# Optimization experiments

Hardware: AMD Instinct MI355X
Metric: run time of the kernel (lower is better)

Reference implementation:

```python
import jax, jax.numpy as jnp
import numpy as np

N_NODES = 100000
N_EDGES = 1600000
D_IN = 64
D_OUT = 64


def setup_inputs() -> dict:
    key = jax.random.key(0)
    k1, k2, k3, k4 = jax.random.split(key, 4)
    x = jax.random.normal(k1, (N_NODES, D_IN), dtype=jnp.float32)
    edge_index = jax.random.randint(k2, (2, N_EDGES), 0, N_NODES, dtype=jnp.int64)
    W = jax.random.normal(k3, (D_OUT, D_IN), dtype=jnp.float32) * (1.0 / np.sqrt(D_IN))
    b = jax.random.normal(k4, (D_OUT,), dtype=jnp.float32) * 0.01
    return {"x": x, "edge_index": edge_index, "W": W, "b": b}


def reference(x, edge_index, W, b):
    num_nodes = x.shape[0]
    row, col = edge_index[0], edge_index[1]
    # degree of each node as a destination (scatter_add of ones over row)
    deg = jax.ops.segment_sum(jnp.ones(row.shape[0], dtype=x.dtype), row,
                              num_segments=num_nodes)
    # deg^-0.5 with inf (deg==0) replaced by 0
    deg_inv_sqrt = jnp.where(deg > 0, jax.lax.rsqrt(jnp.maximum(deg, 1.0)) * jnp.where(deg > 0, 1.0, 0.0), 0.0)
    deg_inv_sqrt = jnp.where(deg > 0, deg ** -0.5, 0.0)
    # gather source features, scale by source norm, scatter-add to destinations
    weighted = x[col] * deg_inv_sqrt[col][:, None]          # [E, D_IN]
    agg = jax.ops.segment_sum(weighted, row, num_segments=num_nodes)  # [N, D_IN]
    agg = agg * deg_inv_sqrt[:, None]
    # linear + relu (torch Linear: y = agg @ W.T + b)
    return jax.nn.relu(agg @ W.T + b)
```

## Files before the change

kernel.cpp:

```cpp
#include <hip/hip_runtime.h>

#define N_NODES 100000
#define N_EDGES 1600000
#define D 64

#define FSHIFT 5
#define FNODES 32
#define NFB 3125
#define CAPF 800

#define CSHIFT 11
#define NCB 49
#define CCAP 36864
#define FPC 64
#define NCHUNKB 9

#define CHUNK 4096
#define EPT 16
#define NCHUNKA 391

#define COLBITS 17
#define COLMASK 0x1FFFF

#define FCUR_OFF   0
#define CCUR_OFF   16384
#define CPAIRS_OFF 32768
#define FPAIRS_OFF 7258112
#define Y_OFF      17258112

typedef float fvec4 __attribute__((ext_vector_type(4)));

__device__ __forceinline__ float bf2f(unsigned short u) {
    return __uint_as_float(((unsigned)u) << 16);
}
__device__ __forceinline__ unsigned f2bf(float f) {
    unsigned bits = __float_as_uint(f);
    return (bits + 0x7FFFu + ((bits >> 16) & 1u)) >> 16;
}

__global__ void initcur_kernel(int* __restrict__ fcur, int* __restrict__ ccur) {
    int i = blockIdx.x * blockDim.x + threadIdx.x;
    if (i < NFB) fcur[i] = i * CAPF;
    if (i < NCB) ccur[i] = i * CCAP;
}

__global__ __launch_bounds__(256) void scatA_kernel(const int* __restrict__ row,
                                                    const int* __restrict__ col,
                                                    int* __restrict__ ccur,
                                                    int* __restrict__ cpairs) {
    __shared__ int lcnt[NCB];
    int t = threadIdx.x;
    int base = blockIdx.x * CHUNK;
    if (t < NCB) lcnt[t] = 0;
    __syncthreads();
    int r[EPT], c[EPT], pos[EPT];
#pragma unroll
    for (int i = 0; i < EPT; ++i) {
        int e = base + i * 256 + t;
        if (e < N_EDGES) {
            r[i] = row[e];
            c[i] = col[e];
            pos[i] = atomicAdd(&lcnt[r[i] >> CSHIFT], 1);
        } else r[i] = -1;
    }
    __syncthreads();
    if (t < NCB) {
        int cc = lcnt[t];
        if (cc) lcnt[t] = atomicAdd(&ccur[t], cc);
    }
    __syncthreads();
#pragma unroll
    for (int i = 0; i < EPT; ++i) {
        if (r[i] >= 0) {
            int cb = r[i] >> CSHIFT;
            int rl = r[i] & ((1 << CSHIFT) - 1);
            cpairs[lcnt[cb] + pos[i]] = (rl << COLBITS) | c[i];
        }
    }
}

__global__ __launch_bounds__(256) void scatB_kernel(const int* __restrict__ cpairs,
                                                    const int* __restrict__ ccur,
                                                    int* __restrict__ fcur,
                                                    int* __restrict__ fpairs) {
    __shared__ int lcnt[FPC];
    int t = threadIdx.x;
    int cb = blockIdx.x / NCHUNKB;
    int k  = blockIdx.x % NCHUNKB;
    int beg = cb * CCAP + k * CHUNK;
    int end = ccur[cb];
    if (end > beg + CHUNK) end = beg + CHUNK;
    if (t < FPC) lcnt[t] = 0;
    __syncthreads();
    int pc[EPT], pos[EPT];
#pragma unroll
    for (int i = 0; i < EPT; ++i) {
        int e = beg + i * 256 + t;
        if (e < end) {
            pc[i] = cpairs[e];
            pos[i] = atomicAdd(&lcnt[pc[i] >> (COLBITS + FSHIFT)], 1);
        } else pc[i] = -1;
    }
    __syncthreads();
    if (t < FPC) {
        int cc = lcnt[t];
        if (cc) lcnt[t] = atomicAdd(&fcur[(cb << 6) + t], cc);
    }
    __syncthreads();
#pragma unroll
    for (int i = 0; i < EPT; ++i) {
        if (pc[i] >= 0) {
            int fl = pc[i] >> (COLBITS + FSHIFT);
            int rl5 = (pc[i] >> COLBITS) & (FNODES - 1);
            fpairs[lcnt[fl] + pos[i]] = (rl5 << COLBITS) | (pc[i] & COLMASK);
        }
    }
}

__global__ __launch_bounds__(256) void xform_kernel(
        const float* __restrict__ x, const float* __restrict__ W,
        const int* __restrict__ fpairs, const int* __restrict__ fcur,
        unsigned short* __restrict__ y) {
    __shared__ __align__(16) float XT[D * 68];
    __shared__ __align__(16) float WT[D * 68];
    __shared__ int hist[64];
    __shared__ float dl[64];
    int t = threadIdx.x;
    int b = blockIdx.x;
    int nb0 = b << 6;
    for (int i = t; i < D * D; i += 256) {
        int j = i >> 6, d = i & 63;
        WT[d * 68 + j] = W[i];
    }
    if (t < 64) hist[t] = 0;
    __syncthreads();
    for (int i = t; i < 64 * D; i += 256) {
        int n = i >> 6, d = i & 63;
        int g = nb0 + n;
        XT[d * 68 + n] = (g < N_NODES) ? x[(size_t)g * D + d] : 0.0f;
    }
#pragma unroll
    for (int half = 0; half < 2; ++half) {
        int f = 2 * b + half;
        if (f < NFB) {
            int beg = f * CAPF, end = fcur[f];
            for (int k = beg + t; k < end; k += 256)
                atomicAdd(&hist[(fpairs[k] >> COLBITS) + (half << FSHIFT)], 1);
        }
    }
    __syncthreads();
    if (t < 64) dl[t] = (hist[t] > 0) ? rsqrtf((float)hist[t]) : 0.0f;
    __syncthreads();
    int tj = t & 15, tn = t >> 4;
    float4 a0 = {0,0,0,0}, a1 = {0,0,0,0}, a2 = {0,0,0,0}, a3 = {0,0,0,0};
#pragma unroll 8
    for (int d = 0; d < D; ++d) {
        float4 xv = *(const float4*)&XT[d * 68 + tn * 4];
        float4 wv = *(const float4*)&WT[d * 68 + tj * 4];
        a0.x = fmaf(xv.x, wv.x, a0.x); a0.y = fmaf(xv.x, wv.y, a0.y);
        a0.z = fmaf(xv.x, wv.z, a0.z); a0.w = fmaf(xv.x, wv.w, a0.w);
        a1.x = fmaf(xv.y, wv.x, a1.x); a1.y = fmaf(xv.y, wv.y, a1.y);
        a1.z = fmaf(xv.y, wv.z, a1.z); a1.w = fmaf(xv.y, wv.w, a1.w);
        a2.x = fmaf(xv.z, wv.x, a2.x); a2.y = fmaf(xv.z, wv.y, a2.y);
        a2.z = fmaf(xv.z, wv.z, a2.z); a2.w = fmaf(xv.z, wv.w, a2.w);
        a3.x = fmaf(xv.w, wv.x, a3.x); a3.y = fmaf(xv.w, wv.y, a3.y);
        a3.z = fmaf(xv.w, wv.z, a3.z); a3.w = fmaf(xv.w, wv.w, a3.w);
    }
    int jb = tj * 4;
#pragma unroll
    for (int s = 0; s < 4; ++s) {
        int g = nb0 + tn * 4 + s;
        if (g < N_NODES) {
            float sc = dl[tn * 4 + s];
            float4 a = (s == 0) ? a0 : (s == 1) ? a1 : (s == 2) ? a2 : a3;
            unsigned lo = f2bf(a.x * sc) | (f2bf(a.y * sc) << 16);
            unsigned hi = f2bf(a.z * sc) | (f2bf(a.w * sc) << 16);
            *(uint2*)(y + (size_t)g * D + jb) = make_uint2(lo, hi);
        }
    }
}

__global__ __launch_bounds__(256) void mega_kernel(
        const int* __restrict__ fpairs, const int* __restrict__ fcur,
        const unsigned short* __restrict__ y,
        const float* __restrict__ bias, float* __restrict__ out) {
    __shared__ int hist[FNODES];
    __shared__ int sc[FNODES];
    __shared__ int lrptr[FNODES + 1];
    __shared__ int lcur[FNODES];
    __shared__ float dl[FNODES];
    __shared__ int lds_scol[CAPF];
    int t = threadIdx.x;
    int b = blockIdx.x;
    int beg = b * CAPF, end = fcur[b];
    if (t < FNODES) hist[t] = 0;
    __syncthreads();
    for (int k = beg + t; k < end; k += 256)
        atomicAdd(&hist[fpairs[k] >> COLBITS], 1);
    __syncthreads();
    if (t < FNODES) sc[t] = hist[t];
    __syncthreads();
    for (int off = 1; off < FNODES; off <<= 1) {
        int v = (t < FNODES && t >= off) ? sc[t - off] : 0;
        __syncthreads();
        if (t < FNODES) sc[t] += v;
        __syncthreads();
    }
    if (t < FNODES) {
        lrptr[t + 1] = sc[t];
        lcur[t] = sc[t] - hist[t];
        dl[t] = (hist[t] > 0) ? rsqrtf((float)hist[t]) : 0.0f;
    }
    if (t == 0) lrptr[0] = 0;
    __syncthreads();
    for (int k = beg + t; k < end; k += 256) {
        int p = fpairs[k];
        int pos = atomicAdd(&lcur[p >> COLBITS], 1);
        lds_scol[pos] = p & COLMASK;
    }
    __syncthreads();
    int wave = t >> 6;
    int lane = t & 63;
    int g = lane >> 3;
    int q = lane & 7;
    float bj[8];
    {
        float4 b0 = *(const float4*)(bias + q * 8);
        float4 b1 = *(const float4*)(bias + q * 8 + 4);
        bj[0] = b0.x; bj[1] = b0.y; bj[2] = b0.z; bj[3] = b0.w;
        bj[4] = b1.x; bj[5] = b1.y; bj[6] = b1.z; bj[7] = b1.w;
    }
    for (int ln = wave; ln < FNODES; ln += 4) {
        int s = lrptr[ln], e2 = lrptr[ln + 1];
        float a[8];
#pragma unroll
        for (int i = 0; i < 8; ++i) a[i] = 0.0f;
        for (int k = s; k < e2; k += 32) {
#pragma unroll
            for (int u = 0; u < 4; ++u) {
                int e = k + u * 8 + g;
                if (e < e2) {
                    int c = lds_scol[e];
                    uint4 v = *(const uint4*)(y + (size_t)c * D + q * 8);
                    a[0] += __uint_as_float(v.x << 16);
                    a[1] += __uint_as_float(v.x & 0xffff0000u);
                    a[2] += __uint_as_float(v.y << 16);
                    a[3] += __uint_as_float(v.y & 0xffff0000u);
                    a[4] += __uint_as_float(v.z << 16);
                    a[5] += __uint_as_float(v.z & 0xffff0000u);
                    a[6] += __uint_as_float(v.w << 16);
                    a[7] += __uint_as_float(v.w & 0xffff0000u);
                }
            }
        }
#pragma unroll
        for (int m = 8; m <= 32; m <<= 1) {
#pragma unroll
            for (int i = 0; i < 8; ++i)
                a[i] += __shfl_xor(a[i], m);
        }
        float dv = dl[ln];
        int n = (b << FSHIFT) + ln;
        if (g < 2) {
            int o = g * 4;
            fvec4 r;
            r.x = fmaxf(fmaf(dv, a[o + 0], bj[o + 0]), 0.0f);
            r.y = fmaxf(fmaf(dv, a[o + 1], bj[o + 1]), 0.0f);
            r.z = fmaxf(fmaf(dv, a[o + 2], bj[o + 2]), 0.0f);
            r.w = fmaxf(fmaf(dv, a[o + 3], bj[o + 3]), 0.0f);
            __builtin_nontemporal_store(r, (fvec4*)(out + (size_t)n * D + q * 8 + o));
        }
    }
}

extern "C" void kernel_launch(void* const* d_in, const int* in_sizes, int n_in,
                              void* d_out, int out_size, void* d_ws, size_t ws_size,
                              hipStream_t stream) {
    const float* x    = (const float*)d_in[0];
    const int*   eidx = (const int*)d_in[1];
    const float* W    = (const float*)d_in[2];
    const float* b    = (const float*)d_in[3];
    float* out = (float*)d_out;
    char* ws = (char*)d_ws;

    const int* row = eidx;
    const int* col = eidx + N_EDGES;

    int* fcur   = (int*)(ws + FCUR_OFF);
    int* ccur   = (int*)(ws + CCUR_OFF);
    int* cpairs = (int*)(ws + CPAIRS_OFF);
    int* fpairs = (int*)(ws + FPAIRS_OFF);
    unsigned short* y = (unsigned short*)(ws + Y_OFF);

    initcur_kernel<<<(NFB + 255) / 256, 256, 0, stream>>>(fcur, ccur);
    scatA_kernel<<<NCHUNKA, 256, 0, stream>>>(row, col, ccur, cpairs);
    scatB_kernel<<<NCB * NCHUNKB, 256, 0, stream>>>(cpairs, ccur, fcur, fpairs);
    xform_kernel<<<(N_NODES + 63) / 64, 256, 0, stream>>>(x, W, fpairs, fcur, y);
    mega_kernel<<<NFB, 256, 0, stream>>>(fpairs, fcur, y, b, out);
}
```

Before: 183.8 us.

## Split feature gather into column planes with a separate CSR prep kernel

```diff
diff --git a/kernel.cpp b/kernel.cpp
--- a/kernel.cpp
+++ b/kernel.cpp
@@ -7,41 +7,39 @@
 #define FSHIFT 5
 #define FNODES 32
 #define NFB 3125
-#define CAPF 800
+#define CAPF 768
 
 #define CSHIFT 11
 #define NCB 49
 #define CCAP 36864
 #define FPC 64
-#define NCHUNKB 9
-
-#define CHUNK 4096
-#define EPT 16
-#define NCHUNKA 391
+
+#define CHUNKA 2048
+#define EPTA 8
+#define NCHUNKA 782
+#define CHUNKB 2048
+#define EPTB 8
+#define NCHUNKB 18
 
 #define COLBITS 17
 #define COLMASK 0x1FFFF
 
-#define FCUR_OFF   0
-#define CCUR_OFF   16384
-#define CPAIRS_OFF 32768
-#define FPAIRS_OFF 7258112
-#define Y_OFF      17258112
+#define PLANE_B 1600000
+
+#define CCUR_OFF   0
+#define FCUR_OFF   4096
+#define INIT_BYTES 16640
+#define RPTR_OFF   16640
+#define DINV_OFF   429312
+#define Y_OFF      829440
+#define FPAIRS_OFF 13629440
+#define SORT_OFF   23229440
 
 typedef float fvec4 __attribute__((ext_vector_type(4)));
 
-__device__ __forceinline__ float bf2f(unsigned short u) {
-    return __uint_as_float(((unsigned)u) << 16);
-}
 __device__ __forceinline__ unsigned f2bf(float f) {
     unsigned bits = __float_as_uint(f);
     return (bits + 0x7FFFu + ((bits >> 16) & 1u)) >> 16;
-}
-
-__global__ void initcur_kernel(int* __restrict__ fcur, int* __restrict__ ccur) {
-    int i = blockIdx.x * blockDim.x + threadIdx.x;
-    if (i < NFB) fcur[i] = i * CAPF;
-    if (i < NCB) ccur[i] = i * CCAP;
 }
 
 __global__ __launch_bounds__(256) void scatA_kernel(const int* __restrict__ row,
@@ -50,12 +48,12 @@
                                                     int* __restrict__ cpairs) {
     __shared__ int lcnt[NCB];
     int t = threadIdx.x;
-    int base = blockIdx.x * CHUNK;
+    int base = blockIdx.x * CHUNKA;
     if (t < NCB) lcnt[t] = 0;
     __syncthreads();
-    int r[EPT], c[EPT], pos[EPT];
-#pragma unroll
-    for (int i = 0; i < EPT; ++i) {
+    int r[EPTA], c[EPTA], pos[EPTA];
+#pragma unroll
+    for (int i = 0; i < EPTA; ++i) {
         int e = base + i * 256 + t;
         if (e < N_EDGES) {
             r[i] = row[e];
@@ -66,11 +64,11 @@
     __syncthreads();
     if (t < NCB) {
         int cc = lcnt[t];
-        if (cc) lcnt[t] = atomicAdd(&ccur[t], cc);
-    }
-    __syncthreads();
-#pragma unroll
-    for (int i = 0; i < EPT; ++i) {
+        if (cc) lcnt[t] = t * CCAP + atomicAdd(&ccur[t], cc);
+    }
+    __syncthreads();
+#pragma unroll
+    for (int i = 0; i < EPTA; ++i) {
         if (r[i] >= 0) {
             int cb = r[i] >> CSHIFT;
             int rl = r[i] & ((1 << CSHIFT) - 1);
@@ -87,14 +85,14 @@
     int t = threadIdx.x;
     int cb = blockIdx.x / NCHUNKB;
     int k  = blockIdx.x % NCHUNKB;
-    int beg = cb * CCAP + k * CHUNK;
-    int end = ccur[cb];
-    if (end > beg + CHUNK) end = beg + CHUNK;
+    int beg = cb * CCAP + k * CHUNKB;
+    int end = cb * CCAP + ccur[cb];
+    if (end > beg + CHUNKB) end = beg + CHUNKB;
     if (t < FPC) lcnt[t] = 0;
     __syncthreads();
-    int pc[EPT], pos[EPT];
-#pragma unroll
-    for (int i = 0; i < EPT; ++i) {
+    int pc[EPTB], pos[EPTB];
+#pragma unroll
+    for (int i = 0; i < EPTB; ++i) {
         int e = beg + i * 256 + t;
         if (e < end) {
             pc[i] = cpairs[e];
@@ -104,11 +102,14 @@
     __syncthreads();
     if (t < FPC) {
         int cc = lcnt[t];
-        if (cc) lcnt[t] = atomicAdd(&fcur[(cb << 6) + t], cc);
-    }
-    __syncthreads();
-#pragma unroll
-    for (int i = 0; i < EPT; ++i) {
+        if (cc) {
+            int fb = (cb << 6) + t;
+            lcnt[t] = fb * CAPF + atomicAdd(&fcur[fb], cc);
+        }
+    }
+    __syncthreads();
+#pragma unroll
+    for (int i = 0; i < EPTB; ++i) {
         if (pc[i] >= 0) {
             int fl = pc[i] >> (COLBITS + FSHIFT);
             int rl5 = (pc[i] >> COLBITS) & (FNODES - 1);
@@ -117,14 +118,55 @@
     }
 }
 
+__global__ __launch_bounds__(256) void binprep_kernel(
+        const int* __restrict__ fpairs, const int* __restrict__ fcur,
+        int* __restrict__ sorted, int* __restrict__ rptr,
+        float* __restrict__ dinv) {
+    __shared__ int hist[FNODES];
+    __shared__ int sc[FNODES];
+    __shared__ int lcur[FNODES];
+    __shared__ int lds_scol[CAPF];
+    int t = threadIdx.x;
+    int f = blockIdx.x;
+    int beg = f * CAPF;
+    int cnt = fcur[f];
+    if (t < FNODES) hist[t] = 0;
+    __syncthreads();
+    for (int k = t; k < cnt; k += 256)
+        atomicAdd(&hist[fpairs[beg + k] >> COLBITS], 1);
+    __syncthreads();
+    if (t < FNODES) sc[t] = hist[t];
+    __syncthreads();
+    for (int off = 1; off < FNODES; off <<= 1) {
+        int v = (t < FNODES && t >= off) ? sc[t - off] : 0;
+        __syncthreads();
+        if (t < FNODES) sc[t] += v;
+        __syncthreads();
+    }
+    if (t < FNODES) {
+        int start = sc[t] - hist[t];
+        lcur[t] = start;
+        rptr[f * 33 + t] = beg + start;
+        int n = (f << FSHIFT) + t;
+        dinv[n] = (hist[t] > 0) ? rsqrtf((float)hist[t]) : 0.0f;
+    }
+    if (t == 0) rptr[f * 33 + 32] = beg + cnt;
+    __syncthreads();
+    for (int k = t; k < cnt; k += 256) {
+        int p = fpairs[beg + k];
+        int pos = atomicAdd(&lcur[p >> COLBITS], 1);
+        lds_scol[pos] = p & COLMASK;
+    }
+    __syncthreads();
+    for (int k = t; k < cnt; k += 256)
+        sorted[beg + k] = lds_scol[k];
+}
+
 __global__ __launch_bounds__(256) void xform_kernel(
         const float* __restrict__ x, const float* __restrict__ W,
-        const int* __restrict__ fpairs, const int* __restrict__ fcur,
-        unsigned short* __restrict__ y) {
+        const float* __restrict__ dinv, char* __restrict__ yb) {
     __shared__ __align__(16) float XT[D * 68];
     __shared__ __align__(16) float WT[D * 68];
-    __shared__ int hist[64];
-    __shared__ float dl[64];
     int t = threadIdx.x;
     int b = blockIdx.x;
     int nb0 = b << 6;
@@ -132,24 +174,11 @@
         int j = i >> 6, d = i & 63;
         WT[d * 68 + j] = W[i];
     }
-    if (t < 64) hist[t] = 0;
-    __syncthreads();
     for (int i = t; i < 64 * D; i += 256) {
         int n = i >> 6, d = i & 63;
         int g = nb0 + n;
         XT[d * 68 + n] = (g < N_NODES) ? x[(size_t)g * D + d] : 0.0f;
     }
-#pragma unroll
-    for (int half = 0; half < 2; ++half) {
-        int f = 2 * b + half;
-        if (f < NFB) {
-            int beg = f * CAPF, end = fcur[f];
-            for (int k = beg + t; k < end; k += 256)
-                atomicAdd(&hist[(fpairs[k] >> COLBITS) + (half << FSHIFT)], 1);
-        }
-    }
-    __syncthreads();
-    if (t < 64) dl[t] = (hist[t] > 0) ? rsqrtf((float)hist[t]) : 0.0f;
     __syncthreads();
     int tj = t & 15, tn = t >> 4;
     float4 a0 = {0,0,0,0}, a1 = {0,0,0,0}, a2 = {0,0,0,0}, a3 = {0,0,0,0};
@@ -166,109 +195,88 @@
         a3.x = fmaf(xv.w, wv.x, a3.x); a3.y = fmaf(xv.w, wv.y, a3.y);
         a3.z = fmaf(xv.w, wv.z, a3.z); a3.w = fmaf(xv.w, wv.w, a3.w);
     }
-    int jb = tj * 4;
+    int p = tj >> 1, half = tj & 1;
 #pragma unroll
     for (int s = 0; s < 4; ++s) {
         int g = nb0 + tn * 4 + s;
         if (g < N_NODES) {
-            float sc = dl[tn * 4 + s];
+            float scv = dinv[g];
             float4 a = (s == 0) ? a0 : (s == 1) ? a1 : (s == 2) ? a2 : a3;
-            unsigned lo = f2bf(a.x * sc) | (f2bf(a.y * sc) << 16);
-            unsigned hi = f2bf(a.z * sc) | (f2bf(a.w * sc) << 16);
-            *(uint2*)(y + (size_t)g * D + jb) = make_uint2(lo, hi);
-        }
-    }
-}
-
-__global__ __launch_bounds__(256) void mega_kernel(
-        const int* __restrict__ fpairs, const int* __restrict__ fcur,
-        const unsigned short* __restrict__ y,
+            unsigned lo = f2bf(a.x * scv) | (f2bf(a.y * scv) << 16);
+            unsigned hi = f2bf(a.z * scv) | (f2bf(a.w * scv) << 16);
+            *(uint2*)(yb + (size_t)p * PLANE_B + (size_t)g * 16 + half * 8) =
+                make_uint2(lo, hi);
+        }
+    }
+}
+
+__global__ __launch_bounds__(256) void gather_kernel(
+        const int* __restrict__ sorted, const int* __restrict__ rptr,
+        const float* __restrict__ dinv, const char* __restrict__ yb,
         const float* __restrict__ bias, float* __restrict__ out) {
-    __shared__ int hist[FNODES];
-    __shared__ int sc[FNODES];
-    __shared__ int lrptr[FNODES + 1];
-    __shared__ int lcur[FNODES];
-    __shared__ float dl[FNODES];
-    __shared__ int lds_scol[CAPF];
-    int t = threadIdx.x;
-    int b = blockIdx.x;
-    int beg = b * CAPF, end = fcur[b];
-    if (t < FNODES) hist[t] = 0;
-    __syncthreads();
-    for (int k = beg + t; k < end; k += 256)
-        atomicAdd(&hist[fpairs[k] >> COLBITS], 1);
-    __syncthreads();
-    if (t < FNODES) sc[t] = hist[t];
-    __syncthreads();
-    for (int off = 1; off < FNODES; off <<= 1) {
-        int v = (t < FNODES && t >= off) ? sc[t - off] : 0;
-        __syncthreads();
-        if (t < FNODES) sc[t] += v;
-        __syncthreads();
-    }
-    if (t < FNODES) {
-        lrptr[t + 1] = sc[t];
-        lcur[t] = sc[t] - hist[t];
-        dl[t] = (hist[t] > 0) ? rsqrtf((float)hist[t]) : 0.0f;
-    }
-    if (t == 0) lrptr[0] = 0;
-    __syncthreads();
-    for (int k = beg + t; k < end; k += 256) {
-        int p = fpairs[k];
-        int pos = atomicAdd(&lcur[p >> COLBITS], 1);
-        lds_scol[pos] = p & COLMASK;
-    }
-    __syncthreads();
-    int wave = t >> 6;
+    int blk = blockIdx.x;
+    int f = blk >> 3;
+    int s = blk & 7;
+    int t = threadIdx.x;
+    int w = t >> 6;
     int lane = t & 63;
-    int g = lane >> 3;
-    int q = lane & 7;
+    int ln2 = lane >> 4;
+    int g = lane & 15;
+    const char* yp = yb + (size_t)s * PLANE_B;
     float bj[8];
     {
-        float4 b0 = *(const float4*)(bias + q * 8);
-        float4 b1 = *(const float4*)(bias + q * 8 + 4);
+        float4 b0 = *(const float4*)(bias + s * 8);
+        float4 b1 = *(const float4*)(bias + s * 8 + 4);
         bj[0] = b0.x; bj[1] = b0.y; bj[2] = b0.z; bj[3] = b0.w;
         bj[4] = b1.x; bj[5] = b1.y; bj[6] = b1.z; bj[7] = b1.w;
     }
-    for (int ln = wave; ln < FNODES; ln += 4) {
-        int s = lrptr[ln], e2 = lrptr[ln + 1];
+    int nb0 = f << FSHIFT;
+#pragma unroll
+    for (int round = 0; round < 2; ++round) {
+        int ln = w * 8 + round * 4 + ln2;
+        int seg = rptr[f * 33 + ln];
+        int deg = rptr[f * 33 + ln + 1] - seg;
+        int md = deg;
+        md = max(md, __shfl_xor(md, 16));
+        md = max(md, __shfl_xor(md, 32));
         float a[8];
 #pragma unroll
         for (int i = 0; i < 8; ++i) a[i] = 0.0f;
-        for (int k = s; k < e2; k += 32) {
-#pragma unroll
-            for (int u = 0; u < 4; ++u) {
-                int e = k + u * 8 + g;
-                if (e < e2) {
-                    int c = lds_scol[e];
-                    uint4 v = *(const uint4*)(y + (size_t)c * D + q * 8);
-                    a[0] += __uint_as_float(v.x << 16);
-                    a[1] += __uint_as_float(v.x & 0xffff0000u);
-                    a[2] += __uint_as_float(v.y << 16);
-                    a[3] += __uint_as_float(v.y & 0xffff0000u);
-                    a[4] += __uint_as_float(v.z << 16);
-                    a[5] += __uint_as_float(v.z & 0xffff0000u);
-                    a[6] += __uint_as_float(v.w << 16);
-                    a[7] += __uint_as_float(v.w & 0xffff0000u);
-                }
+        for (int base = 0; base < md; base += 16) {
+            int o = base + g;
+            if (o < deg) {
+                int c = sorted[seg + o];
+                uint4 v = *(const uint4*)(yp + (size_t)c * 16);
+                a[0] += __uint_as_float(v.x << 16);
+                a[1] += __uint_as_float(v.x & 0xffff0000u);
+                a[2] += __uint_as_float(v.y << 16);
+                a[3] += __uint_as_float(v.y & 0xffff0000u);
+                a[4] += __uint_as_float(v.z << 16);
+                a[5] += __uint_as_float(v.z & 0xffff0000u);
+                a[6] += __uint_as_float(v.w << 16);
+                a[7] += __uint_as_float(v.w & 0xffff0000u);
             }
         }
 #pragma unroll
-        for (int m = 8; m <= 32; m <<= 1) {
+        for (int m = 1; m <= 8; m <<= 1) {
 #pragma unroll
             for (int i = 0; i < 8; ++i)
                 a[i] += __shfl_xor(a[i], m);
         }
-        float dv = dl[ln];
-        int n = (b << FSHIFT) + ln;
-        if (g < 2) {
-            int o = g * 4;
-            fvec4 r;
-            r.x = fmaxf(fmaf(dv, a[o + 0], bj[o + 0]), 0.0f);
-            r.y = fmaxf(fmaf(dv, a[o + 1], bj[o + 1]), 0.0f);
-            r.z = fmaxf(fmaf(dv, a[o + 2], bj[o + 2]), 0.0f);
-            r.w = fmaxf(fmaf(dv, a[o + 3], bj[o + 3]), 0.0f);
-            __builtin_nontemporal_store(r, (fvec4*)(out + (size_t)n * D + q * 8 + o));
+        if (g == 0) {
+            int n = nb0 + ln;
+            float dv = dinv[n];
+            fvec4 r0, r1;
+            r0.x = fmaxf(fmaf(dv, a[0], bj[0]), 0.0f);
+            r0.y = fmaxf(fmaf(dv, a[1], bj[1]), 0.0f);
+            r0.z = fmaxf(fmaf(dv, a[2], bj[2]), 0.0f);
+            r0.w = fmaxf(fmaf(dv, a[3], bj[3]), 0.0f);
+            r1.x = fmaxf(fmaf(dv, a[4], bj[4]), 0.0f);
+            r1.y = fmaxf(fmaf(dv, a[5], bj[5]), 0.0f);
+            r1.z = fmaxf(fmaf(dv, a[6], bj[6]), 0.0f);
+            r1.w = fmaxf(fmaf(dv, a[7], bj[7]), 0.0f);
+            __builtin_nontemporal_store(r0, (fvec4*)(out + (size_t)n * D + s * 8));
+            __builtin_nontemporal_store(r1, (fvec4*)(out + (size_t)n * D + s * 8 + 4));
         }
     }
 }
@@ -286,15 +294,19 @@
     const int* row = eidx;
     const int* col = eidx + N_EDGES;
 
-    int* fcur   = (int*)(ws + FCUR_OFF);
-    int* ccur   = (int*)(ws + CCUR_OFF);
-    int* cpairs = (int*)(ws + CPAIRS_OFF);
-    int* fpairs = (int*)(ws + FPAIRS_OFF);
-    unsigned short* y = (unsigned short*)(ws + Y_OFF);
-
-    initcur_kernel<<<(NFB + 255) / 256, 256, 0, stream>>>(fcur, ccur);
+    int*   ccur   = (int*)  (ws + CCUR_OFF);
+    int*   fcur   = (int*)  (ws + FCUR_OFF);
+    int*   rptr   = (int*)  (ws + RPTR_OFF);
+    float* dinv   = (float*)(ws + DINV_OFF);
+    char*  yb     =          ws + Y_OFF;
+    int*   fpairs = (int*)  (ws + FPAIRS_OFF);
+    int*   sorted = (int*)  (ws + SORT_OFF);
+    int*   cpairs = (int*)  (ws + SORT_OFF);
+
+    hipMemsetAsync(ws + CCUR_OFF, 0, INIT_BYTES, stream);
     scatA_kernel<<<NCHUNKA, 256, 0, stream>>>(row, col, ccur, cpairs);
     scatB_kernel<<<NCB * NCHUNKB, 256, 0, stream>>>(cpairs, ccur, fcur, fpairs);
-    xform_kernel<<<(N_NODES + 63) / 64, 256, 0, stream>>>(x, W, fpairs, fcur, y);
-    mega_kernel<<<NFB, 256, 0, stream>>>(fpairs, fcur, y, b, out);
-}
+    binprep_kernel<<<NFB, 256, 0, stream>>>(fpairs, fcur, sorted, rptr, dinv);
+    xform_kernel<<<(N_NODES + 63) / 64, 256, 0, stream>>>(x, W, dinv, yb);
+    gather_kernel<<<NFB * 8, 256, 0, stream>>>(sorted, rptr, dinv, yb, b, out);
+}
```

Result: slower. 240.6 us (+30.9%).

## Compute degree norms in scatter pass and split binning counters per wave

Applied to the files above, without the earlier changes.

```diff
diff --git a/kernel.cpp b/kernel.cpp
--- a/kernel.cpp
+++ b/kernel.cpp
@@ -7,123 +7,155 @@
 #define FSHIFT 5
 #define FNODES 32
 #define NFB 3125
-#define CAPF 800
+#define CAPF 768
 
 #define CSHIFT 11
+#define CNODES 2048
 #define NCB 49
 #define CCAP 36864
 #define FPC 64
-#define NCHUNKB 9
-
-#define CHUNK 4096
-#define EPT 16
+
+#define CHUNKA 4096
+#define EPTA 16
 #define NCHUNKA 391
+#define CHUNKB 2048
+#define EPTB 8
+#define NCHUNKB 18
 
 #define COLBITS 17
 #define COLMASK 0x1FFFF
 
-#define FCUR_OFF   0
-#define CCUR_OFF   16384
-#define CPAIRS_OFF 32768
-#define FPAIRS_OFF 7258112
-#define Y_OFF      17258112
+#define CCUR_OFF   0
+#define FCUR_OFF   256
+#define INIT_BYTES 12756
+#define DINV_OFF   16384
+#define Y_OFF      417792
+#define CPAIRS_OFF 13217792
+#define FPAIRS_OFF 20443136
 
 typedef float fvec4 __attribute__((ext_vector_type(4)));
 
-__device__ __forceinline__ float bf2f(unsigned short u) {
-    return __uint_as_float(((unsigned)u) << 16);
-}
 __device__ __forceinline__ unsigned f2bf(float f) {
     unsigned bits = __float_as_uint(f);
     return (bits + 0x7FFFu + ((bits >> 16) & 1u)) >> 16;
-}
-
-__global__ void initcur_kernel(int* __restrict__ fcur, int* __restrict__ ccur) {
-    int i = blockIdx.x * blockDim.x + threadIdx.x;
-    if (i < NFB) fcur[i] = i * CAPF;
-    if (i < NCB) ccur[i] = i * CCAP;
 }
 
 __global__ __launch_bounds__(256) void scatA_kernel(const int* __restrict__ row,
                                                     const int* __restrict__ col,
                                                     int* __restrict__ ccur,
                                                     int* __restrict__ cpairs) {
-    __shared__ int lcnt[NCB];
+    __shared__ int lcnt[4][52];
+    __shared__ int wbase[4][52];
     int t = threadIdx.x;
-    int base = blockIdx.x * CHUNK;
-    if (t < NCB) lcnt[t] = 0;
-    __syncthreads();
-    int r[EPT], c[EPT], pos[EPT];
-#pragma unroll
-    for (int i = 0; i < EPT; ++i) {
+    int w = t >> 6;
+    int base = blockIdx.x * CHUNKA;
+    for (int i = t; i < 4 * 52; i += 256) ((int*)lcnt)[i] = 0;
+    __syncthreads();
+    int r[EPTA], c[EPTA], pos[EPTA];
+#pragma unroll
+    for (int i = 0; i < EPTA; ++i) {
         int e = base + i * 256 + t;
         if (e < N_EDGES) {
             r[i] = row[e];
             c[i] = col[e];
-            pos[i] = atomicAdd(&lcnt[r[i] >> CSHIFT], 1);
+            pos[i] = atomicAdd(&lcnt[w][r[i] >> CSHIFT], 1);
         } else r[i] = -1;
     }
     __syncthreads();
     if (t < NCB) {
-        int cc = lcnt[t];
-        if (cc) lcnt[t] = atomicAdd(&ccur[t], cc);
-    }
-    __syncthreads();
-#pragma unroll
-    for (int i = 0; i < EPT; ++i) {
+        int c0 = lcnt[0][t], c1 = lcnt[1][t], c2 = lcnt[2][t], c3 = lcnt[3][t];
+        int tot = c0 + c1 + c2 + c3;
+        int g = t * CCAP;
+        if (tot) g += atomicAdd(&ccur[t], tot);
+        wbase[0][t] = g;
+        wbase[1][t] = g + c0;
+        wbase[2][t] = g + c0 + c1;
+        wbase[3][t] = g + c0 + c1 + c2;
+    }
+    __syncthreads();
+#pragma unroll
+    for (int i = 0; i < EPTA; ++i) {
         if (r[i] >= 0) {
             int cb = r[i] >> CSHIFT;
-            int rl = r[i] & ((1 << CSHIFT) - 1);
-            cpairs[lcnt[cb] + pos[i]] = (rl << COLBITS) | c[i];
-        }
-    }
-}
-
-__global__ __launch_bounds__(256) void scatB_kernel(const int* __restrict__ cpairs,
-                                                    const int* __restrict__ ccur,
-                                                    int* __restrict__ fcur,
-                                                    int* __restrict__ fpairs) {
-    __shared__ int lcnt[FPC];
+            int rl = r[i] & (CNODES - 1);
+            cpairs[wbase[w][cb] + pos[i]] = (rl << COLBITS) | c[i];
+        }
+    }
+}
+
+__global__ __launch_bounds__(256) void scatB_dinv_kernel(
+        const int* __restrict__ cpairs, const int* __restrict__ ccur,
+        int* __restrict__ fcur, int* __restrict__ fpairs,
+        float* __restrict__ dinv) {
+    __shared__ int hist[CNODES];
+    __shared__ int lcnt[4][FPC];
+    __shared__ int wbase[4][FPC];
     int t = threadIdx.x;
-    int cb = blockIdx.x / NCHUNKB;
-    int k  = blockIdx.x % NCHUNKB;
-    int beg = cb * CCAP + k * CHUNK;
-    int end = ccur[cb];
-    if (end > beg + CHUNK) end = beg + CHUNK;
-    if (t < FPC) lcnt[t] = 0;
-    __syncthreads();
-    int pc[EPT], pos[EPT];
-#pragma unroll
-    for (int i = 0; i < EPT; ++i) {
+    int blk = blockIdx.x;
+    if (blk < NCB) {
+        int cb = blk;
+        int beg = cb * CCAP;
+        int end = beg + ccur[cb];
+        for (int i = t; i < CNODES; i += 256) hist[i] = 0;
+        __syncthreads();
+        for (int k = beg + t; k < end; k += 256)
+            atomicAdd(&hist[cpairs[k] >> COLBITS], 1);
+        __syncthreads();
+        for (int i = t; i < CNODES; i += 256) {
+            int n = (cb << CSHIFT) + i;
+            if (n < N_NODES) {
+                int d = hist[i];
+                dinv[n] = (d > 0) ? rsqrtf((float)d) : 0.0f;
+            }
+        }
+        return;
+    }
+    int w = t >> 6;
+    int bb = blk - NCB;
+    int cb = bb / NCHUNKB;
+    int k  = bb % NCHUNKB;
+    int beg = cb * CCAP + k * CHUNKB;
+    int end = cb * CCAP + ccur[cb];
+    if (end > beg + CHUNKB) end = beg + CHUNKB;
+    for (int i = t; i < 4 * FPC; i += 256) ((int*)lcnt)[i] = 0;
+    __syncthreads();
+    int pc[EPTB], pos[EPTB];
+#pragma unroll
+    for (int i = 0; i < EPTB; ++i) {
         int e = beg + i * 256 + t;
         if (e < end) {
             pc[i] = cpairs[e];
-            pos[i] = atomicAdd(&lcnt[pc[i] >> (COLBITS + FSHIFT)], 1);
+            pos[i] = atomicAdd(&lcnt[w][pc[i] >> (COLBITS + FSHIFT)], 1);
         } else pc[i] = -1;
     }
     __syncthreads();
     if (t < FPC) {
-        int cc = lcnt[t];
-        if (cc) lcnt[t] = atomicAdd(&fcur[(cb << 6) + t], cc);
-    }
-    __syncthreads();
-#pragma unroll
-    for (int i = 0; i < EPT; ++i) {
+        int c0 = lcnt[0][t], c1 = lcnt[1][t], c2 = lcnt[2][t], c3 = lcnt[3][t];
+        int tot = c0 + c1 + c2 + c3;
+        int fb = (cb << 6) + t;
+        int g = fb * CAPF;
+        if (tot) g += atomicAdd(&fcur[fb], tot);
+        wbase[0][t] = g;
+        wbase[1][t] = g + c0;
+        wbase[2][t] = g + c0 + c1;
+        wbase[3][t] = g + c0 + c1 + c2;
+    }
+    __syncthreads();
+#pragma unroll
+    for (int i = 0; i < EPTB; ++i) {
         if (pc[i] >= 0) {
             int fl = pc[i] >> (COLBITS + FSHIFT);
             int rl5 = (pc[i] >> COLBITS) & (FNODES - 1);
-            fpairs[lcnt[fl] + pos[i]] = (rl5 << COLBITS) | (pc[i] & COLMASK);
+            fpairs[wbase[w][fl] + pos[i]] = (rl5 << COLBITS) | (pc[i] & COLMASK);
         }
     }
 }
 
 __global__ __launch_bounds__(256) void xform_kernel(
         const float* __restrict__ x, const float* __restrict__ W,
-        const int* __restrict__ fpairs, const int* __restrict__ fcur,
-        unsigned short* __restrict__ y) {
+        const float* __restrict__ dinv, unsigned short* __restrict__ y) {
     __shared__ __align__(16) float XT[D * 68];
     __shared__ __align__(16) float WT[D * 68];
-    __shared__ int hist[64];
     __shared__ float dl[64];
     int t = threadIdx.x;
     int b = blockIdx.x;
@@ -132,24 +164,15 @@
         int j = i >> 6, d = i & 63;
         WT[d * 68 + j] = W[i];
     }
-    if (t < 64) hist[t] = 0;
-    __syncthreads();
+    if (t < 64) {
+        int g = nb0 + t;
+        dl[t] = (g < N_NODES) ? dinv[g] : 0.0f;
+    }
     for (int i = t; i < 64 * D; i += 256) {
         int n = i >> 6, d = i & 63;
         int g = nb0 + n;
         XT[d * 68 + n] = (g < N_NODES) ? x[(size_t)g * D + d] : 0.0f;
     }
-#pragma unroll
-    for (int half = 0; half < 2; ++half) {
-        int f = 2 * b + half;
-        if (f < NFB) {
-            int beg = f * CAPF, end = fcur[f];
-            for (int k = beg + t; k < end; k += 256)
-                atomicAdd(&hist[(fpairs[k] >> COLBITS) + (half << FSHIFT)], 1);
-        }
-    }
-    __syncthreads();
-    if (t < 64) dl[t] = (hist[t] > 0) ? rsqrtf((float)hist[t]) : 0.0f;
     __syncthreads();
     int tj = t & 15, tn = t >> 4;
     float4 a0 = {0,0,0,0}, a1 = {0,0,0,0}, a2 = {0,0,0,0}, a3 = {0,0,0,0};
@@ -171,10 +194,10 @@
     for (int s = 0; s < 4; ++s) {
         int g = nb0 + tn * 4 + s;
         if (g < N_NODES) {
-            float sc = dl[tn * 4 + s];
+            float scv = dl[tn * 4 + s];
             float4 a = (s == 0) ? a0 : (s == 1) ? a1 : (s == 2) ? a2 : a3;
-            unsigned lo = f2bf(a.x * sc) | (f2bf(a.y * sc) << 16);
-            unsigned hi = f2bf(a.z * sc) | (f2bf(a.w * sc) << 16);
+            unsigned lo = f2bf(a.x * scv) | (f2bf(a.y * scv) << 16);
+            unsigned hi = f2bf(a.z * scv) | (f2bf(a.w * scv) << 16);
             *(uint2*)(y + (size_t)g * D + jb) = make_uint2(lo, hi);
         }
     }
@@ -192,11 +215,12 @@
     __shared__ int lds_scol[CAPF];
     int t = threadIdx.x;
     int b = blockIdx.x;
-    int beg = b * CAPF, end = fcur[b];
+    int beg = b * CAPF;
+    int cnt = fcur[b];
     if (t < FNODES) hist[t] = 0;
     __syncthreads();
-    for (int k = beg + t; k < end; k += 256)
-        atomicAdd(&hist[fpairs[k] >> COLBITS], 1);
+    for (int k = t; k < cnt; k += 256)
+        atomicAdd(&hist[fpairs[beg + k] >> COLBITS], 1);
     __syncthreads();
     if (t < FNODES) sc[t] = hist[t];
     __syncthreads();
@@ -213,8 +237,8 @@
     }
     if (t == 0) lrptr[0] = 0;
     __syncthreads();
-    for (int k = beg + t; k < end; k += 256) {
-        int p = fpairs[k];
+    for (int k = t; k < cnt; k += 256) {
+        int p = fpairs[beg + k];
         int pos = atomicAdd(&lcur[p >> COLBITS], 1);
         lds_scol[pos] = p & COLMASK;
     }
@@ -286,15 +310,16 @@
     const int* row = eidx;
     const int* col = eidx + N_EDGES;
 
-    int* fcur   = (int*)(ws + FCUR_OFF);
-    int* ccur   = (int*)(ws + CCUR_OFF);
-    int* cpairs = (int*)(ws + CPAIRS_OFF);
-    int* fpairs = (int*)(ws + FPAIRS_OFF);
+    int*   ccur   = (int*)  (ws + CCUR_OFF);
+    int*   fcur   = (int*)  (ws + FCUR_OFF);
+    float* dinv   = (float*)(ws + DINV_OFF);
     unsigned short* y = (unsigned short*)(ws + Y_OFF);
-
-    initcur_kernel<<<(NFB + 255) / 256, 256, 0, stream>>>(fcur, ccur);
+    int*   cpairs = (int*)  (ws + CPAIRS_OFF);
+    int*   fpairs = (int*)  (ws + FPAIRS_OFF);
+
+    hipMemsetAsync(ws, 0, INIT_BYTES, stream);
     scatA_kernel<<<NCHUNKA, 256, 0, stream>>>(row, col, ccur, cpairs);
-    scatB_kernel<<<NCB * NCHUNKB, 256, 0, stream>>>(cpairs, ccur, fcur, fpairs);
-    xform_kernel<<<(N_NODES + 63) / 64, 256, 0, stream>>>(x, W, fpairs, fcur, y);
+    scatB_dinv_kernel<<<NCB + NCB * NCHUNKB, 256, 0, stream>>>(cpairs, ccur, fcur, fpairs, dinv);
+    xform_kernel<<<(N_NODES + 63) / 64, 256, 0, stream>>>(x, W, dinv, y);
     mega_kernel<<<NFB, 256, 0, stream>>>(fpairs, fcur, y, b, out);
 }
```

New measurement: 207.6 us. 1.13x slower.
